# Kernel tuning notes

Measured on AMD Instinct MI355X. Metric: run time of the kernel, lower is better.

Reference implementation:

```python
import jax, jax.numpy as jnp
import numpy as np

N = 50000      # nodes
E = 800000     # edges (avg degree 16)
D_IN, D_H, D_OUT = 128, 128, 64
BN_EPS = 1e-5


def setup_inputs() -> dict:
    key = jax.random.key(0)
    ks = jax.random.split(key, 16)
    rn = lambda k, shape, s=0.05: (jax.random.normal(k, shape, jnp.float32) * s)
    inp = {
        'x': jax.random.normal(ks[0], (N, D_IN), jnp.float32),
        'edge_index': jax.random.randint(ks[1], (2, E), 0, N, jnp.int64),
        # layer 0: SAGEConv(D_IN -> D_H): lin_l (neighbors, bias), lin_r (self, no bias)
        'W0l': rn(ks[2], (D_IN, D_H)), 'W0r': rn(ks[3], (D_IN, D_H)), 'b0': jnp.zeros((D_H,), jnp.float32),
        'g0': jnp.ones((D_H,), jnp.float32), 'be0': jnp.zeros((D_H,), jnp.float32),
        # layer 1: SAGEConv(D_H -> D_H)
        'W1l': rn(ks[4], (D_H, D_H)), 'W1r': rn(ks[5], (D_H, D_H)), 'b1': jnp.zeros((D_H,), jnp.float32),
        'g1': jnp.ones((D_H,), jnp.float32), 'be1': jnp.zeros((D_H,), jnp.float32),
        # layer 2: SAGEConv(D_H -> D_OUT)
        'W2l': rn(ks[6], (D_H, D_OUT)), 'W2r': rn(ks[7], (D_H, D_OUT)), 'b2': jnp.zeros((D_OUT,), jnp.float32),
    }
    return inp


def _sage_conv(x, src, dst, Wl, Wr, b):
    # aggr='add': sum neighbor features x[src] into dst, then linear; self path via Wr
    agg = jax.ops.segment_sum(x[src], dst, num_segments=N)  # [N, D]
    return agg @ Wl + x @ Wr + b


def _batchnorm(h, gamma, beta):
    mu = jnp.mean(h, axis=0)
    var = jnp.var(h, axis=0)
    return (h - mu) * jax.lax.rsqrt(var + BN_EPS) * gamma + beta


def reference(x, edge_index, W0l, W0r, b0, g0, be0, W1l, W1r, b1, g1, be1, W2l, W2r, b2):
    src, dst = edge_index[0], edge_index[1]
    # layer 0: conv -> BN -> GELU (dropout is identity at eval)
    h = _sage_conv(x, src, dst, W0l, W0r, b0)
    h = jax.nn.gelu(_batchnorm(h, g0, be0), approximate=False)
    # layer 1
    h = _sage_conv(h, src, dst, W1l, W1r, b1)
    h = jax.nn.gelu(_batchnorm(h, g1, be1), approximate=False)
    # final layer: conv only
    return _sage_conv(h, src, dst, W2l, W2r, b2)
```

## Files before the change

kernel.cpp:

```cpp
#include <hip/hip_runtime.h>
#include <math.h>

#define NN 50000
#define DEGCAP 64

typedef unsigned short u16;
typedef short bf16x8 __attribute__((ext_vector_type(8)));
typedef float floatx4 __attribute__((ext_vector_type(4)));

__device__ inline u16 f32_to_bf16(float f) {
  unsigned u = __builtin_bit_cast(unsigned, f);
  u += 0x7fffu + ((u >> 16) & 1u);
  return (u16)(u >> 16);
}
__device__ inline float bf16_to_f32(u16 h) {
  unsigned u = ((unsigned)h) << 16;
  return __builtin_bit_cast(float, u);
}
__device__ inline float gelu_exact(float v) {
  return 0.5f * v * (1.0f + erff(v * 0.70710678118654752f));
}

__global__ __launch_bounds__(256) void setup_kernel(
    const float* W0l, const float* W0r, const float* W1l,
    const float* W1r, const float* W2l, const float* W2r,
    u16* __restrict__ Wt, int* __restrict__ cnt, float* __restrict__ stats, int n) {
  int b = blockIdx.x;
  if (b < 6) {
    const float* src;
    int ncols;
    switch (b) {
      case 0: src = W0l; ncols = 128; break;
      case 1: src = W0r; ncols = 128; break;
      case 2: src = W1l; ncols = 128; break;
      case 3: src = W1r; ncols = 128; break;
      case 4: src = W2l; ncols = 64; break;
      default: src = W2r; ncols = 64; break;
    }
    u16* dst = Wt + b * 16384;
    int total = ncols * 128;
    for (int idx = threadIdx.x; idx < total; idx += 256) {
      int nc = idx >> 7, kk = idx & 127;
      dst[nc * 128 + kk] = f32_to_bf16(src[kk * ncols + nc]);
    }
  } else {
    int i = (b - 6) * 256 + threadIdx.x;
    if (i < n) cnt[i] = 0;
    if (b == 6) { stats[threadIdx.x] = 0.0f; stats[256 + threadIdx.x] = 0.0f; }
  }
}

__global__ void fill_kernel(const int* __restrict__ src, const int* __restrict__ dst,
                            int* __restrict__ cnt, u16* __restrict__ ssrc, int E) {
  int e = blockIdx.x * blockDim.x + threadIdx.x;
  if (e < E) {
    int d = dst[e];
    int p = atomicAdd(&cnt[d], 1);
    if (p < DEGCAP) ssrc[d * DEGCAP + p] = (u16)src[e];
  }
}

#define LOAD_CVT 0
#define LOAD_BN  1
template <int NL, int NR, int MODE>
__global__ __launch_bounds__(256, 2) void gemm_dual_kernel(
    const float* __restrict__ A, const u16* __restrict__ WtL, const u16* __restrict__ WtR,
    const float* __restrict__ bias, const float* __restrict__ stats,
    const float* __restrict__ g, const float* __restrict__ be,
    u16* __restrict__ Cl, float* __restrict__ Cr, int n) {
  constexpr int NTOT = NL + NR;
  constexpr int NT = NTOT / 16;
  constexpr int NTL = NL / 16;
  __shared__ u16 Wlds[NTOT * 128];
  __shared__ float sc_s[128], sh_s[128];
  int t = threadIdx.x;

  if (MODE == LOAD_BN && t < 128) {
    float inv_n = 1.0f / (float)NN;
    float mu = stats[t] * inv_n;
    float var = stats[128 + t] * inv_n - mu * mu;
    float s = rsqrtf(var + 1e-5f) * g[t];
    sc_s[t] = s;
    sh_s[t] = be[t] - mu * s;
  }
  for (int idx = t; idx < NTOT * 16; idx += 256) {
    int rw = idx >> 4, c = idx & 15;
    const u16* srcp = (rw < NL) ? (WtL + rw * 128 + c * 8) : (WtR + (rw - NL) * 128 + c * 8);
    *(float4*)(&Wlds[rw * 128 + ((c ^ (rw & 15)) * 8)]) = *(const float4*)srcp;
  }
  __syncthreads();

  int wave = t >> 6, lane = t & 63;
  int quad = lane >> 4, l16 = lane & 15;
  int row0 = blockIdx.x * 128 + wave * 32;
  int ar0 = row0 + l16, ar1 = row0 + 16 + l16;
  bool ok0 = ar0 < n, ok1 = ar1 < n;
  const float* Ap0 = A + (size_t)ar0 * 128 + quad * 8;
  const float* Ap1 = A + (size_t)ar1 * 128 + quad * 8;

  floatx4 acc0[NT], acc1[NT];
#pragma unroll
  for (int i = 0; i < NT; i++) {
    acc0[i] = (floatx4){0.f, 0.f, 0.f, 0.f};
    acc1[i] = (floatx4){0.f, 0.f, 0.f, 0.f};
  }

#pragma unroll
  for (int kk = 0; kk < 4; kk++) {
    bf16x8 a0, a1;
    {
      float vv[16];
      if (ok0) {
        float4 f0 = *(const float4*)(Ap0 + kk * 32);
        float4 f1 = *(const float4*)(Ap0 + kk * 32 + 4);
        vv[0] = f0.x; vv[1] = f0.y; vv[2] = f0.z; vv[3] = f0.w;
        vv[4] = f1.x; vv[5] = f1.y; vv[6] = f1.z; vv[7] = f1.w;
      } else {
#pragma unroll
        for (int j = 0; j < 8; j++) vv[j] = 0.f;
      }
      if (ok1) {
        float4 f0 = *(const float4*)(Ap1 + kk * 32);
        float4 f1 = *(const float4*)(Ap1 + kk * 32 + 4);
        vv[8] = f0.x; vv[9] = f0.y; vv[10] = f0.z; vv[11] = f0.w;
        vv[12] = f1.x; vv[13] = f1.y; vv[14] = f1.z; vv[15] = f1.w;
      } else {
#pragma unroll
        for (int j = 8; j < 16; j++) vv[j] = 0.f;
      }
      if (MODE == LOAD_BN) {
        int kb = kk * 32 + quad * 8;
#pragma unroll
        for (int j = 0; j < 8; j++) {
          float sc = sc_s[kb + j], sh = sh_s[kb + j];
          if (ok0) vv[j] = gelu_exact(vv[j] * sc + sh);
          if (ok1) vv[8 + j] = gelu_exact(vv[8 + j] * sc + sh);
        }
      }
#pragma unroll
      for (int j = 0; j < 8; j++) {
        a0[j] = (short)f32_to_bf16(vv[j]);
        a1[j] = (short)f32_to_bf16(vv[8 + j]);
      }
    }
    int chunk8 = ((kk * 4 + quad) ^ l16) * 8;
    const u16* wp = &Wlds[l16 * 128 + chunk8];
#pragma unroll
    for (int tile = 0; tile < NT; tile++) {
      bf16x8 b = *(const bf16x8*)(wp + tile * 2048);
      acc0[tile] = __builtin_amdgcn_mfma_f32_16x16x32_bf16(a0, b, acc0[tile], 0, 0, 0);
      acc1[tile] = __builtin_amdgcn_mfma_f32_16x16x32_bf16(a1, b, acc1[tile], 0, 0, 0);
    }
  }

#pragma unroll
  for (int tile = 0; tile < NT; tile++) {
#pragma unroll
    for (int r = 0; r < 4; r++) {
      int rowA = row0 + quad * 4 + r;
      int rowB = rowA + 16;
      if (tile < NTL) {
        int col = tile * 16 + l16;
        if (rowA < n) Cl[(size_t)rowA * NL + col] = f32_to_bf16(acc0[tile][r]);
        if (rowB < n) Cl[(size_t)rowB * NL + col] = f32_to_bf16(acc1[tile][r]);
      } else {
        int col = (tile - NTL) * 16 + l16;
        float bv = bias[col];
        if (rowA < n) Cr[(size_t)rowA * NR + col] = acc0[tile][r] + bv;
        if (rowB < n) Cr[(size_t)rowB * NR + col] = acc1[tile][r] + bv;
      }
    }
  }
}

template <int D>
__global__ __launch_bounds__(256) void aggregate_kernel(
    const u16* __restrict__ yl, const int* __restrict__ cnt,
    const u16* __restrict__ ssrc, float* __restrict__ h, int n) {
  constexpr int TPN = D / 4;
  constexpr int NPB = 256 / TPN;
  int node = blockIdx.x * NPB + threadIdx.x / TPN;
  int c4 = (threadIdx.x % TPN) * 4;
  if (node >= n) return;
  int deg = cnt[node]; if (deg > DEGCAP) deg = DEGCAP;
  const u16* sp = ssrc + (size_t)node * DEGCAP;
  float4 acc = *(const float4*)(h + (size_t)node * D + c4);
  int j = 0;
  for (; j + 7 < deg; j += 8) {
    int s0 = sp[j], s1 = sp[j + 1], s2 = sp[j + 2], s3 = sp[j + 3];
    int s4 = sp[j + 4], s5 = sp[j + 5], s6 = sp[j + 6], s7 = sp[j + 7];
    ushort4 v0 = *(const ushort4*)(yl + (size_t)s0 * D + c4);
    ushort4 v1 = *(const ushort4*)(yl + (size_t)s1 * D + c4);
    ushort4 v2 = *(const ushort4*)(yl + (size_t)s2 * D + c4);
    ushort4 v3 = *(const ushort4*)(yl + (size_t)s3 * D + c4);
    ushort4 v4 = *(const ushort4*)(yl + (size_t)s4 * D + c4);
    ushort4 v5 = *(const ushort4*)(yl + (size_t)s5 * D + c4);
    ushort4 v6 = *(const ushort4*)(yl + (size_t)s6 * D + c4);
    ushort4 v7 = *(const ushort4*)(yl + (size_t)s7 * D + c4);
    acc.x += bf16_to_f32(v0.x) + bf16_to_f32(v1.x) + bf16_to_f32(v2.x) + bf16_to_f32(v3.x)
           + bf16_to_f32(v4.x) + bf16_to_f32(v5.x) + bf16_to_f32(v6.x) + bf16_to_f32(v7.x);
    acc.y += bf16_to_f32(v0.y) + bf16_to_f32(v1.y) + bf16_to_f32(v2.y) + bf16_to_f32(v3.y)
           + bf16_to_f32(v4.y) + bf16_to_f32(v5.y) + bf16_to_f32(v6.y) + bf16_to_f32(v7.y);
    acc.z += bf16_to_f32(v0.z) + bf16_to_f32(v1.z) + bf16_to_f32(v2.z) + bf16_to_f32(v3.z)
           + bf16_to_f32(v4.z) + bf16_to_f32(v5.z) + bf16_to_f32(v6.z) + bf16_to_f32(v7.z);
    acc.w += bf16_to_f32(v0.w) + bf16_to_f32(v1.w) + bf16_to_f32(v2.w) + bf16_to_f32(v3.w)
           + bf16_to_f32(v4.w) + bf16_to_f32(v5.w) + bf16_to_f32(v6.w) + bf16_to_f32(v7.w);
  }
  for (; j < deg; j++) {
    int s0 = sp[j];
    ushort4 v0 = *(const ushort4*)(yl + (size_t)s0 * D + c4);
    acc.x += bf16_to_f32(v0.x); acc.y += bf16_to_f32(v0.y);
    acc.z += bf16_to_f32(v0.z); acc.w += bf16_to_f32(v0.w);
  }
  *(float4*)(h + (size_t)node * D + c4) = acc;
}

__global__ __launch_bounds__(256) void bnstats_kernel(
    const float* __restrict__ h, float* __restrict__ stats, int n) {
  int c = threadIdx.x & 127;
  int half = threadIdx.x >> 7;
  float sum = 0.f, sq = 0.f;
  for (int r = blockIdx.x * 2 + half; r < n; r += gridDim.x * 2) {
    float v = h[(size_t)r * 128 + c];
    sum += v; sq += v * v;
  }
  __shared__ float ls[256], lq[256];
  ls[threadIdx.x] = sum; lq[threadIdx.x] = sq;
  __syncthreads();
  if (threadIdx.x < 128) {
    sum = ls[threadIdx.x] + ls[threadIdx.x + 128];
    sq = lq[threadIdx.x] + lq[threadIdx.x + 128];
    atomicAdd(&stats[c], sum);
    atomicAdd(&stats[128 + c], sq);
  }
}

extern "C" void kernel_launch(void* const* d_in, const int* in_sizes, int n_in,
                              void* d_out, int out_size, void* d_ws, size_t ws_size,
                              hipStream_t stream) {
  const float* x   = (const float*)d_in[0];
  const int* edge  = (const int*)d_in[1];
  const int E = in_sizes[1] / 2;
  const int* esrc = edge;
  const int* edst = edge + E;
  const float* W0l = (const float*)d_in[2];
  const float* W0r = (const float*)d_in[3];
  const float* b0  = (const float*)d_in[4];
  const float* g0  = (const float*)d_in[5];
  const float* be0 = (const float*)d_in[6];
  const float* W1l = (const float*)d_in[7];
  const float* W1r = (const float*)d_in[8];
  const float* b1  = (const float*)d_in[9];
  const float* g1  = (const float*)d_in[10];
  const float* be1 = (const float*)d_in[11];
  const float* W2l = (const float*)d_in[12];
  const float* W2r = (const float*)d_in[13];
  const float* b2  = (const float*)d_in[14];
  float* out = (float*)d_out;

  const int n = NN;
  int* cnt   = (int*)d_ws;
  float* stats = (float*)(cnt + 50000);
  u16* ssrc  = (u16*)(stats + 512);
  u16* Wt    = ssrc + (size_t)NN * DEGCAP;
  u16* ylb   = Wt + 6 * 16384;
  float* ha  = (float*)(ylb + (size_t)n * 128);
  float* hb  = ha + (size_t)n * 128;
  float* stats0 = stats;
  float* stats1 = stats + 256;

  const int TB = 256;
  const int NB1 = (n + 255) / 256;

  setup_kernel<<<6 + NB1, TB, 0, stream>>>(W0l, W0r, W1l, W1r, W2l, W2r, Wt, cnt, stats, n);
  fill_kernel<<<(E + TB - 1) / TB, TB, 0, stream>>>(esrc, edst, cnt, ssrc, E);

  const int GB = (n + 127) / 128;

  gemm_dual_kernel<128, 128, LOAD_CVT><<<GB, TB, 0, stream>>>(
      x, Wt + 0 * 16384, Wt + 1 * 16384, b0, nullptr, nullptr, nullptr, ylb, ha, n);
  aggregate_kernel<128><<<(n + 7) / 8, TB, 0, stream>>>(ylb, cnt, ssrc, ha, n);
  bnstats_kernel<<<256, TB, 0, stream>>>(ha, stats0, n);

  gemm_dual_kernel<128, 128, LOAD_BN><<<GB, TB, 0, stream>>>(
      ha, Wt + 2 * 16384, Wt + 3 * 16384, b1, stats0, g0, be0, ylb, hb, n);
  aggregate_kernel<128><<<(n + 7) / 8, TB, 0, stream>>>(ylb, cnt, ssrc, hb, n);
  bnstats_kernel<<<256, TB, 0, stream>>>(hb, stats1, n);

  gemm_dual_kernel<64, 64, LOAD_BN><<<GB, TB, 0, stream>>>(
      hb, Wt + 4 * 16384, Wt + 5 * 16384, b2, stats1, g1, be1, ylb, out, n);
  aggregate_kernel<64><<<(n + 15) / 16, TB, 0, stream>>>(ylb, cnt, ssrc, out, n);
}
```

Before: 403.4 us.

## Store hidden activations in bf16 and widen gather loads to 8 elements

Intermediate hidden buffers (self-path GEMM output, aggregated h) switch from fp32 to bf16, so the GEMM, aggregate and BN-stats kernels read and write half the bytes. The aggregate kernel now has each thread handle 8 channels with 16-byte bf16x8 gathers, and its unroll drops from 8 to 4. The fill kernel processes two edges per thread with int2 loads. Rounding the hidden state to bf16 adds some accuracy loss in the BN statistics and the pre-activation values.

```diff
diff --git a/kernel.cpp b/kernel.cpp
--- a/kernel.cpp
+++ b/kernel.cpp
@@ -52,8 +52,15 @@
 
 __global__ void fill_kernel(const int* __restrict__ src, const int* __restrict__ dst,
                             int* __restrict__ cnt, u16* __restrict__ ssrc, int E) {
-  int e = blockIdx.x * blockDim.x + threadIdx.x;
-  if (e < E) {
+  int e = (blockIdx.x * blockDim.x + threadIdx.x) * 2;
+  if (e + 1 < E) {
+    int2 s = *(const int2*)(src + e);
+    int2 d = *(const int2*)(dst + e);
+    int p0 = atomicAdd(&cnt[d.x], 1);
+    int p1 = atomicAdd(&cnt[d.y], 1);
+    if (p0 < DEGCAP) ssrc[d.x * DEGCAP + p0] = (u16)s.x;
+    if (p1 < DEGCAP) ssrc[d.y * DEGCAP + p1] = (u16)s.y;
+  } else if (e < E) {
     int d = dst[e];
     int p = atomicAdd(&cnt[d], 1);
     if (p < DEGCAP) ssrc[d * DEGCAP + p] = (u16)src[e];
@@ -62,12 +69,12 @@
 
 #define LOAD_CVT 0
 #define LOAD_BN  1
-template <int NL, int NR, int MODE>
+template <int NL, int NR, int MODE, bool CRF>
 __global__ __launch_bounds__(256, 2) void gemm_dual_kernel(
-    const float* __restrict__ A, const u16* __restrict__ WtL, const u16* __restrict__ WtR,
+    const void* __restrict__ Av, const u16* __restrict__ WtL, const u16* __restrict__ WtR,
     const float* __restrict__ bias, const float* __restrict__ stats,
     const float* __restrict__ g, const float* __restrict__ be,
-    u16* __restrict__ Cl, float* __restrict__ Cr, int n) {
+    u16* __restrict__ Cl, void* __restrict__ Crv, int n) {
   constexpr int NTOT = NL + NR;
   constexpr int NT = NTOT / 16;
   constexpr int NTL = NL / 16;
@@ -95,8 +102,6 @@
   int row0 = blockIdx.x * 128 + wave * 32;
   int ar0 = row0 + l16, ar1 = row0 + 16 + l16;
   bool ok0 = ar0 < n, ok1 = ar1 < n;
-  const float* Ap0 = A + (size_t)ar0 * 128 + quad * 8;
-  const float* Ap1 = A + (size_t)ar1 * 128 + quad * 8;
 
   floatx4 acc0[NT], acc1[NT];
 #pragma unroll
@@ -110,23 +115,38 @@
     bf16x8 a0, a1;
     {
       float vv[16];
-      if (ok0) {
-        float4 f0 = *(const float4*)(Ap0 + kk * 32);
-        float4 f1 = *(const float4*)(Ap0 + kk * 32 + 4);
-        vv[0] = f0.x; vv[1] = f0.y; vv[2] = f0.z; vv[3] = f0.w;
-        vv[4] = f1.x; vv[5] = f1.y; vv[6] = f1.z; vv[7] = f1.w;
+      if (MODE == LOAD_CVT) {
+        const float* A = (const float*)Av;
+        const float* Ap0 = A + (size_t)ar0 * 128 + quad * 8 + kk * 32;
+        const float* Ap1 = A + (size_t)ar1 * 128 + quad * 8 + kk * 32;
+        if (ok0) {
+          float4 f0 = *(const float4*)(Ap0);
+          float4 f1 = *(const float4*)(Ap0 + 4);
+          vv[0] = f0.x; vv[1] = f0.y; vv[2] = f0.z; vv[3] = f0.w;
+          vv[4] = f1.x; vv[5] = f1.y; vv[6] = f1.z; vv[7] = f1.w;
+        } else {
+#pragma unroll
+          for (int j = 0; j < 8; j++) vv[j] = 0.f;
+        }
+        if (ok1) {
+          float4 f0 = *(const float4*)(Ap1);
+          float4 f1 = *(const float4*)(Ap1 + 4);
+          vv[8] = f0.x; vv[9] = f0.y; vv[10] = f0.z; vv[11] = f0.w;
+          vv[12] = f1.x; vv[13] = f1.y; vv[14] = f1.z; vv[15] = f1.w;
+        } else {
+#pragma unroll
+          for (int j = 8; j < 16; j++) vv[j] = 0.f;
+        }
       } else {
-#pragma unroll
-        for (int j = 0; j < 8; j++) vv[j] = 0.f;
-      }
-      if (ok1) {
-        float4 f0 = *(const float4*)(Ap1 + kk * 32);
-        float4 f1 = *(const float4*)(Ap1 + kk * 32 + 4);
-        vv[8] = f0.x; vv[9] = f0.y; vv[10] = f0.z; vv[11] = f0.w;
-        vv[12] = f1.x; vv[13] = f1.y; vv[14] = f1.z; vv[15] = f1.w;
-      } else {
-#pragma unroll
-        for (int j = 8; j < 16; j++) vv[j] = 0.f;
+        const u16* A = (const u16*)Av;
+        bf16x8 r0 = (bf16x8){0,0,0,0,0,0,0,0}, r1 = r0;
+        if (ok0) r0 = *(const bf16x8*)(A + (size_t)ar0 * 128 + quad * 8 + kk * 32);
+        if (ok1) r1 = *(const bf16x8*)(A + (size_t)ar1 * 128 + quad * 8 + kk * 32);
+#pragma unroll
+        for (int j = 0; j < 8; j++) {
+          vv[j] = bf16_to_f32((u16)r0[j]);
+          vv[8 + j] = bf16_to_f32((u16)r1[j]);
+        }
       }
       if (MODE == LOAD_BN) {
         int kb = kk * 32 + quad * 8;
@@ -166,62 +186,87 @@
       } else {
         int col = (tile - NTL) * 16 + l16;
         float bv = bias[col];
-        if (rowA < n) Cr[(size_t)rowA * NR + col] = acc0[tile][r] + bv;
-        if (rowB < n) Cr[(size_t)rowB * NR + col] = acc1[tile][r] + bv;
+        if (CRF) {
+          float* Cr = (float*)Crv;
+          if (rowA < n) Cr[(size_t)rowA * NR + col] = acc0[tile][r] + bv;
+          if (rowB < n) Cr[(size_t)rowB * NR + col] = acc1[tile][r] + bv;
+        } else {
+          u16* Cr = (u16*)Crv;
+          if (rowA < n) Cr[(size_t)rowA * NR + col] = f32_to_bf16(acc0[tile][r] + bv);
+          if (rowB < n) Cr[(size_t)rowB * NR + col] = f32_to_bf16(acc1[tile][r] + bv);
+        }
       }
     }
   }
 }
 
-template <int D>
+template <int D, bool HF>
 __global__ __launch_bounds__(256) void aggregate_kernel(
     const u16* __restrict__ yl, const int* __restrict__ cnt,
-    const u16* __restrict__ ssrc, float* __restrict__ h, int n) {
-  constexpr int TPN = D / 4;
+    const u16* __restrict__ ssrc, void* __restrict__ hv, int n) {
+  constexpr int TPN = D / 8;
   constexpr int NPB = 256 / TPN;
   int node = blockIdx.x * NPB + threadIdx.x / TPN;
-  int c4 = (threadIdx.x % TPN) * 4;
+  int c8 = (threadIdx.x % TPN) * 8;
   if (node >= n) return;
   int deg = cnt[node]; if (deg > DEGCAP) deg = DEGCAP;
   const u16* sp = ssrc + (size_t)node * DEGCAP;
-  float4 acc = *(const float4*)(h + (size_t)node * D + c4);
+
+  float acc[8];
+  if (HF) {
+    float* h = (float*)hv + (size_t)node * D + c8;
+    float4 h0 = *(const float4*)(h);
+    float4 h1 = *(const float4*)(h + 4);
+    acc[0] = h0.x; acc[1] = h0.y; acc[2] = h0.z; acc[3] = h0.w;
+    acc[4] = h1.x; acc[5] = h1.y; acc[6] = h1.z; acc[7] = h1.w;
+  } else {
+    const u16* h = (const u16*)hv + (size_t)node * D + c8;
+    bf16x8 hb = *(const bf16x8*)h;
+#pragma unroll
+    for (int q = 0; q < 8; q++) acc[q] = bf16_to_f32((u16)hb[q]);
+  }
+
   int j = 0;
-  for (; j + 7 < deg; j += 8) {
+  for (; j + 3 < deg; j += 4) {
     int s0 = sp[j], s1 = sp[j + 1], s2 = sp[j + 2], s3 = sp[j + 3];
-    int s4 = sp[j + 4], s5 = sp[j + 5], s6 = sp[j + 6], s7 = sp[j + 7];
-    ushort4 v0 = *(const ushort4*)(yl + (size_t)s0 * D + c4);
-    ushort4 v1 = *(const ushort4*)(yl + (size_t)s1 * D + c4);
-    ushort4 v2 = *(const ushort4*)(yl + (size_t)s2 * D + c4);
-    ushort4 v3 = *(const ushort4*)(yl + (size_t)s3 * D + c4);
-    ushort4 v4 = *(const ushort4*)(yl + (size_t)s4 * D + c4);
-    ushort4 v5 = *(const ushort4*)(yl + (size_t)s5 * D + c4);
-    ushort4 v6 = *(const ushort4*)(yl + (size_t)s6 * D + c4);
-    ushort4 v7 = *(const ushort4*)(yl + (size_t)s7 * D + c4);
-    acc.x += bf16_to_f32(v0.x) + bf16_to_f32(v1.x) + bf16_to_f32(v2.x) + bf16_to_f32(v3.x)
-           + bf16_to_f32(v4.x) + bf16_to_f32(v5.x) + bf16_to_f32(v6.x) + bf16_to_f32(v7.x);
-    acc.y += bf16_to_f32(v0.y) + bf16_to_f32(v1.y) + bf16_to_f32(v2.y) + bf16_to_f32(v3.y)
-           + bf16_to_f32(v4.y) + bf16_to_f32(v5.y) + bf16_to_f32(v6.y) + bf16_to_f32(v7.y);
-    acc.z += bf16_to_f32(v0.z) + bf16_to_f32(v1.z) + bf16_to_f32(v2.z) + bf16_to_f32(v3.z)
-           + bf16_to_f32(v4.z) + bf16_to_f32(v5.z) + bf16_to_f32(v6.z) + bf16_to_f32(v7.z);
-    acc.w += bf16_to_f32(v0.w) + bf16_to_f32(v1.w) + bf16_to_f32(v2.w) + bf16_to_f32(v3.w)
-           + bf16_to_f32(v4.w) + bf16_to_f32(v5.w) + bf16_to_f32(v6.w) + bf16_to_f32(v7.w);
+    bf16x8 v0 = *(const bf16x8*)(yl + (size_t)s0 * D + c8);
+    bf16x8 v1 = *(const bf16x8*)(yl + (size_t)s1 * D + c8);
+    bf16x8 v2 = *(const bf16x8*)(yl + (size_t)s2 * D + c8);
+    bf16x8 v3 = *(const bf16x8*)(yl + (size_t)s3 * D + c8);
+#pragma unroll
+    for (int q = 0; q < 8; q++)
+      acc[q] += bf16_to_f32((u16)v0[q]) + bf16_to_f32((u16)v1[q])
+              + bf16_to_f32((u16)v2[q]) + bf16_to_f32((u16)v3[q]);
   }
   for (; j < deg; j++) {
     int s0 = sp[j];
-    ushort4 v0 = *(const ushort4*)(yl + (size_t)s0 * D + c4);
-    acc.x += bf16_to_f32(v0.x); acc.y += bf16_to_f32(v0.y);
-    acc.z += bf16_to_f32(v0.z); acc.w += bf16_to_f32(v0.w);
-  }
-  *(float4*)(h + (size_t)node * D + c4) = acc;
+    bf16x8 v0 = *(const bf16x8*)(yl + (size_t)s0 * D + c8);
+#pragma unroll
+    for (int q = 0; q < 8; q++) acc[q] += bf16_to_f32((u16)v0[q]);
+  }
+
+  if (HF) {
+    float* h = (float*)hv + (size_t)node * D + c8;
+    float4 o0 = {acc[0], acc[1], acc[2], acc[3]};
+    float4 o1 = {acc[4], acc[5], acc[6], acc[7]};
+    *(float4*)(h) = o0;
+    *(float4*)(h + 4) = o1;
+  } else {
+    u16* h = (u16*)hv + (size_t)node * D + c8;
+    bf16x8 o;
+#pragma unroll
+    for (int q = 0; q < 8; q++) o[q] = (short)f32_to_bf16(acc[q]);
+    *(bf16x8*)h = o;
+  }
 }
 
 __global__ __launch_bounds__(256) void bnstats_kernel(
-    const float* __restrict__ h, float* __restrict__ stats, int n) {
+    const u16* __restrict__ h, float* __restrict__ stats, int n) {
   int c = threadIdx.x & 127;
   int half = threadIdx.x >> 7;
   float sum = 0.f, sq = 0.f;
   for (int r = blockIdx.x * 2 + half; r < n; r += gridDim.x * 2) {
-    float v = h[(size_t)r * 128 + c];
+    float v = bf16_to_f32(h[(size_t)r * 128 + c]);
     sum += v; sq += v * v;
   }
   __shared__ float ls[256], lq[256];
@@ -264,8 +309,8 @@
   u16* ssrc  = (u16*)(stats + 512);
   u16* Wt    = ssrc + (size_t)NN * DEGCAP;
   u16* ylb   = Wt + 6 * 16384;
-  float* ha  = (float*)(ylb + (size_t)n * 128);
-  float* hb  = ha + (size_t)n * 128;
+  u16* ha    = ylb + (size_t)n * 128;
+  u16* hb    = ha + (size_t)n * 128;
   float* stats0 = stats;
   float* stats1 = stats + 256;
 
@@ -273,21 +318,21 @@
   const int NB1 = (n + 255) / 256;
 
   setup_kernel<<<6 + NB1, TB, 0, stream>>>(W0l, W0r, W1l, W1r, W2l, W2r, Wt, cnt, stats, n);
-  fill_kernel<<<(E + TB - 1) / TB, TB, 0, stream>>>(esrc, edst, cnt, ssrc, E);
+  fill_kernel<<<(E / 2 + TB - 1) / TB, TB, 0, stream>>>(esrc, edst, cnt, ssrc, E);
 
   const int GB = (n + 127) / 128;
 
-  gemm_dual_kernel<128, 128, LOAD_CVT><<<GB, TB, 0, stream>>>(
+  gemm_dual_kernel<128, 128, LOAD_CVT, false><<<GB, TB, 0, stream>>>(
       x, Wt + 0 * 16384, Wt + 1 * 16384, b0, nullptr, nullptr, nullptr, ylb, ha, n);
-  aggregate_kernel<128><<<(n + 7) / 8, TB, 0, stream>>>(ylb, cnt, ssrc, ha, n);
+  aggregate_kernel<128, false><<<(n + 15) / 16, TB, 0, stream>>>(ylb, cnt, ssrc, ha, n);
   bnstats_kernel<<<256, TB, 0, stream>>>(ha, stats0, n);
 
-  gemm_dual_kernel<128, 128, LOAD_BN><<<GB, TB, 0, stream>>>(
+  gemm_dual_kernel<128, 128, LOAD_BN, false><<<GB, TB, 0, stream>>>(
       ha, Wt + 2 * 16384, Wt + 3 * 16384, b1, stats0, g0, be0, ylb, hb, n);
-  aggregate_kernel<128><<<(n + 7) / 8, TB, 0, stream>>>(ylb, cnt, ssrc, hb, n);
+  aggregate_kernel<128, false><<<(n + 15) / 16, TB, 0, stream>>>(ylb, cnt, ssrc, hb, n);
   bnstats_kernel<<<256, TB, 0, stream>>>(hb, stats1, n);
 
-  gemm_dual_kernel<64, 64, LOAD_BN><<<GB, TB, 0, stream>>>(
+  gemm_dual_kernel<64, 64, LOAD_BN, true><<<GB, TB, 0, stream>>>(
       hb, Wt + 4 * 16384, Wt + 5 * 16384, b2, stats1, g1, be1, ylb, out, n);
-  aggregate_kernel<64><<<(n + 15) / 16, TB, 0, stream>>>(ylb, cnt, ssrc, out, n);
-}
+  aggregate_kernel<64, true><<<(n + 31) / 32, TB, 0, stream>>>(ylb, cnt, ssrc, out, n);
+}
```

After: 387.5 us. 3.9% less time.
